# Performance work log

Measured on AMD Instinct MI355X. Metric: run time of the kernel, lower is better.

The kernel has to match this reference:

```python
import jax, jax.numpy as jnp
import numpy as np

HIDDEN_SIZE = 256
INPUT_SIZE = 4
N_CLASSES = 2


def setup_inputs() -> dict:
    key = jax.random.key(0)
    ks = jax.random.split(key, 12)
    B, T, H, I = 64, 2048, HIDDEN_SIZE, INPUT_SIZE
    s = 0.1
    return {
        "y": jax.random.normal(ks[0], (B, T), dtype=jnp.float32),
        "W_ih0": s * jax.random.normal(ks[1], (4 * H, I), dtype=jnp.float32),
        "W_hh0": s * jax.random.normal(ks[2], (4 * H, H), dtype=jnp.float32),
        "b_ih0": s * jax.random.normal(ks[3], (4 * H,), dtype=jnp.float32),
        "b_hh0": s * jax.random.normal(ks[4], (4 * H,), dtype=jnp.float32),
        "W_ih1": s * jax.random.normal(ks[5], (4 * H, H), dtype=jnp.float32),
        "W_hh1": s * jax.random.normal(ks[6], (4 * H, H), dtype=jnp.float32),
        "b_ih1": s * jax.random.normal(ks[7], (4 * H,), dtype=jnp.float32),
        "b_hh1": s * jax.random.normal(ks[8], (4 * H,), dtype=jnp.float32),
        "W_fc": s * jax.random.normal(ks[9], (N_CLASSES, H), dtype=jnp.float32),
        "b_fc": s * jax.random.normal(ks[10], (N_CLASSES,), dtype=jnp.float32),
    }


def _lstm_cell(x, h, c, Wi, Wh, bi, bh):
    # gate order i, f, g, o (torch convention, matches explicit slicing)
    gates = x @ Wi.T + bi + h @ Wh.T + bh  # [B, 4H]
    i, f, g, o = jnp.split(gates, 4, axis=-1)
    c_new = jax.nn.sigmoid(f) * c + jax.nn.sigmoid(i) * jnp.tanh(g)
    h_new = jax.nn.sigmoid(o) * jnp.tanh(c_new)
    return h_new, c_new


def reference(y, W_ih0, W_hh0, b_ih0, b_hh0, W_ih1, W_hh1, b_ih1, b_hh1, W_fc, b_fc):
    B, T = y.shape
    H = HIDDEN_SIZE
    # Sliding-window input: window [y[t-3], y[t-2], y[t-1], y[t]] with -100 pad
    padded = jnp.pad(y, ((0, 0), (0, INPUT_SIZE - 1)), constant_values=-100.0)
    seq = jnp.stack([jnp.roll(padded, s, axis=1) for s in range(INPUT_SIZE - 1, -1, -1)], axis=-1)
    seq = seq[:, :T]  # [B, T, 4]

    def step(carry, x_t):
        h0, c0, h1, c1 = carry
        h0, c0 = _lstm_cell(x_t, h0, c0, W_ih0, W_hh0, b_ih0, b_hh0)
        h1, c1 = _lstm_cell(h0, h1, c1, W_ih1, W_hh1, b_ih1, b_hh1)
        return (h0, c0, h1, c1), h1

    z = jnp.zeros((B, H), dtype=y.dtype)
    _, hs = jax.lax.scan(step, (z, z, z, z), jnp.swapaxes(seq, 0, 1))  # hs: [T, B, H]
    lstm_out = jnp.swapaxes(hs, 0, 1)  # [B, T, H]
    out = lstm_out @ W_fc.T + b_fc  # [B, T, N_CLASSES]
    return out
```

## Files before the change

kernel.cpp:

```cpp
#include <hip/hip_runtime.h>


#define NWG 64
#define NSTRIP 32
#define BB 64
#define TT 2048
#define HH 256
#define HS 8
#define HSW 4
#define RS 16

#define WS_H0    0
#define WS_H1    16384
#define WS_FLAGS 32768
#define WS_CNT   33792
#define WS_WIN   33808
#define WS_NZERO 33808

typedef float  f32x4  __attribute__((ext_vector_type(4)));
typedef __bf16 bf16x8 __attribute__((ext_vector_type(8)));
typedef unsigned long long u64;
typedef unsigned int u32;

__device__ __forceinline__ float sigf(float x)   { return 1.0f / (1.0f + __expf(-x)); }
__device__ __forceinline__ float tanh_f(float x) { return 2.0f / (1.0f + __expf(-2.0f * x)) - 1.0f; }

__global__ void init_ws(u32* ws) {
  int i = blockIdx.x * blockDim.x + threadIdx.x;
  for (; i < WS_NZERO; i += gridDim.x * blockDim.x) ws[i] = 0u;
  if (blockIdx.x == 0 && threadIdx.x == 0) ((int*)ws)[WS_WIN] = -1;
}

__global__ __launch_bounds__(256, 2) void lstm2_persistent(
    const float* __restrict__ y,
    const float* __restrict__ Wih0, const float* __restrict__ Whh0,
    const float* __restrict__ bih0, const float* __restrict__ bhh0,
    const float* __restrict__ Wih1, const float* __restrict__ Whh1,
    const float* __restrict__ bih1, const float* __restrict__ bhh1,
    const float* __restrict__ Wfc,  const float* __restrict__ bfc,
    float* __restrict__ out,
    u32* __restrict__ ws)
{
  __bf16* h0buf = (__bf16*)(ws + WS_H0);
  __bf16* h1buf = (__bf16*)(ws + WS_H1);
  int*    flags = (int*)(ws + WS_FLAGS);
  int*    cnt   = (int*)(ws + WS_CNT);
  int*    winner= (int*)(ws + WS_WIN);

  const int tid  = threadIdx.x;

  __shared__ int s_w;
  if (tid == 0) {
    int xcc = __builtin_amdgcn_s_getreg(20 | (31 << 11)) & 0xF;
    int r = atomicAdd(&cnt[xcc], 1);
    if (r == NWG - 1) atomicCAS(winner, -1, xcc);
    int wv;
    while ((wv = __hip_atomic_load(winner, __ATOMIC_RELAXED,
                                   __HIP_MEMORY_SCOPE_AGENT)) == -1) {}
    s_w = (wv == xcc && r < NWG) ? r : -1;
  }
  __syncthreads();
  const int w = s_w;
  if (w < 0) return;

  const int wave = tid >> 6;
  const int lane = tid & 63;
  const int ml   = lane & 15;
  const int kq   = lane >> 4;

  __shared__ float lds_g0[RS][BB + 4];
  __shared__ float lds_g1[RS][BB + 4];
  __shared__ float s_wih0[RS][4];
  __shared__ float s_b0[RS];
  __shared__ float s_b1[RS];

  bf16x8 w0f[8];
  bf16x8 w1f[16];
  {
    const int r     = ml;
    const int rglob = (r >> 2) * 256 + w * HSW + (r & 3);
    #pragma unroll
    for (int s = 0; s < 8; s++) {
      const float* src = Whh0 + rglob * HH + s * 32 + kq * 8;
      bf16x8 f;
      #pragma unroll
      for (int j = 0; j < 8; j++) f[j] = (__bf16)src[j];
      w0f[s] = f;
    }
    #pragma unroll
    for (int s = 0; s < 16; s++) {
      const int k = s * 32 + kq * 8;
      const float* src = (k < 256) ? (Wih1 + rglob * HH + k)
                                   : (Whh1 + rglob * HH + (k - 256));
      bf16x8 f;
      #pragma unroll
      for (int j = 0; j < 8; j++) f[j] = (__bf16)src[j];
      w1f[s] = f;
    }
  }

  if (tid < RS) {
    const int r     = tid;
    const int rglob = (r >> 2) * 256 + w * HSW + (r & 3);
    s_b0[r] = bih0[rglob] + bhh0[rglob];
    s_b1[r] = bih1[rglob] + bhh1[rglob];
    #pragma unroll
    for (int j = 0; j < 4; j++) s_wih0[r][j] = Wih0[rglob * 4 + j];
  }
  __syncthreads();

  float c0 = 0.f, c1 = 0.f;

  const int b_epi = tid >> 2;
  const int dl    = tid & 3;

  float x[4] = {-100.0f, -100.0f, -100.0f, -100.0f};

  for (int p = 0; p < TT + 2; p++) {
    const int par  = p & 1;
    const int parm = par ^ 1;

    const bool doL0 = (p < TT);
    const bool doL1 = (p >= 1 && p <= TT);

    bf16x8 a0[8], a1[8];
    {
      const int row = wave * 16 + ml;
      const __bf16* h0p = h0buf + (parm * NSTRIP * BB + kq * BB + row) * HS;
      const __bf16* h1p = h1buf + (par  * NSTRIP * BB + kq * BB + row) * HS;
      #pragma unroll
      for (int s = 0; s < 8; s++)
        asm volatile("global_load_dwordx4 %0, %1, off sc0"
                     : "=v"(a0[s]) : "v"(h0p + s * 4 * BB * HS) : "memory");
      #pragma unroll
      for (int s = 0; s < 8; s++)
        asm volatile("global_load_dwordx4 %0, %1, off sc0"
                     : "=v"(a1[s]) : "v"(h1p + s * 4 * BB * HS) : "memory");
    }

    x[0] = x[1]; x[1] = x[2]; x[2] = x[3];
    x[3] = (p < TT) ? y[b_epi * TT + p] : -100.0f;

    asm volatile("s_waitcnt vmcnt(0)" ::: "memory");
    __builtin_amdgcn_sched_barrier(0);

    f32x4 acc0  = {0.f,0.f,0.f,0.f};
    f32x4 acc1a = {0.f,0.f,0.f,0.f};
    f32x4 acc1b = {0.f,0.f,0.f,0.f};

    if (doL0) {
      #pragma unroll
      for (int s = 0; s < 8; s++)
        acc0 = __builtin_amdgcn_mfma_f32_16x16x32_bf16(a0[s], w0f[s], acc0, 0, 0, 0);
    }
    if (doL1) {
      #pragma unroll
      for (int s = 0; s < 8; s++)
        acc1a = __builtin_amdgcn_mfma_f32_16x16x32_bf16(a0[s], w1f[s], acc1a, 0, 0, 0);
      #pragma unroll
      for (int s = 0; s < 8; s++)
        acc1b = __builtin_amdgcn_mfma_f32_16x16x32_bf16(a1[s], w1f[s + 8], acc1b, 0, 0, 0);
    }

    {
      const int bb = wave * 16 + kq * 4;
      if (doL0) {
        #pragma unroll
        for (int j = 0; j < 4; j++) lds_g0[ml][bb + j] = acc0[j];
      }
      if (doL1) {
        #pragma unroll
        for (int j = 0; j < 4; j++) lds_g1[ml][bb + j] = acc1a[j] + acc1b[j];
      }
    }
    __syncthreads();

    if (doL0) {
      const float gi = lds_g0[dl     ][b_epi] + s_b0[dl     ]
        + s_wih0[dl     ][0]*x[0] + s_wih0[dl     ][1]*x[1] + s_wih0[dl     ][2]*x[2] + s_wih0[dl     ][3]*x[3];
      const float gf = lds_g0[4 + dl ][b_epi] + s_b0[4 + dl ]
        + s_wih0[4 + dl ][0]*x[0] + s_wih0[4 + dl ][1]*x[1] + s_wih0[4 + dl ][2]*x[2] + s_wih0[4 + dl ][3]*x[3];
      const float gg = lds_g0[8 + dl ][b_epi] + s_b0[8 + dl ]
        + s_wih0[8 + dl ][0]*x[0] + s_wih0[8 + dl ][1]*x[1] + s_wih0[8 + dl ][2]*x[2] + s_wih0[8 + dl ][3]*x[3];
      const float go = lds_g0[12 + dl][b_epi] + s_b0[12 + dl]
        + s_wih0[12 + dl][0]*x[0] + s_wih0[12 + dl][1]*x[1] + s_wih0[12 + dl][2]*x[2] + s_wih0[12 + dl][3]*x[3];
      const float cn = sigf(gf) * c0 + sigf(gi) * tanh_f(gg);
      c0 = cn;
      const float hn = sigf(go) * tanh_f(cn);
      h0buf[(par * NSTRIP * BB + (w >> 1) * BB + b_epi) * HS + (w & 1) * 4 + dl] = (__bf16)hn;
    }

    if (doL1) {
      const float gi = lds_g1[dl     ][b_epi] + s_b1[dl     ];
      const float gf = lds_g1[4 + dl ][b_epi] + s_b1[4 + dl ];
      const float gg = lds_g1[8 + dl ][b_epi] + s_b1[8 + dl ];
      const float go = lds_g1[12 + dl][b_epi] + s_b1[12 + dl];
      const float cn = sigf(gf) * c1 + sigf(gi) * tanh_f(gg);
      c1 = cn;
      const float hn = sigf(go) * tanh_f(cn);
      h1buf[(parm * NSTRIP * BB + (w >> 1) * BB + b_epi) * HS + (w & 1) * 4 + dl] = (__bf16)hn;
    }

    asm volatile("s_waitcnt vmcnt(0)" ::: "memory");
    __syncthreads();
    if (tid == 0)
      __hip_atomic_store(&flags[w * 16], p + 2, __ATOMIC_RELAXED,
                         __HIP_MEMORY_SCOPE_WORKGROUP);

    if (p >= 2 && wave < 2) {
      const int t = p - 2;
      const int b = w;
      const int c = wave;
      const __bf16* h1r = h1buf + (par * NSTRIP * BB + (lane >> 1) * BB + b) * HS + (lane & 1) * 4;
      union { u64 u; __bf16 h[4]; } c4;
      c4.u = __hip_atomic_load((u64*)h1r, __ATOMIC_RELAXED,
                               __HIP_MEMORY_SCOPE_AGENT);
      float s = 0.f;
      #pragma unroll
      for (int j = 0; j < 4; j++)
        s += (float)c4.h[j] * Wfc[c * HH + lane * 4 + j];
      #pragma unroll
      for (int off = 32; off > 0; off >>= 1) s += __shfl_down(s, off, 64);
      if (lane == 0) out[b * (TT * 2) + t * 2 + c] = s + bfc[c];
    }

    if (tid < NWG) {
      while (__hip_atomic_load(&flags[tid * 16], __ATOMIC_RELAXED,
                               __HIP_MEMORY_SCOPE_AGENT) < p + 2) {}
    }
    __syncthreads();
  }
}

extern "C" void kernel_launch(void* const* d_in, const int* in_sizes, int n_in,
                              void* d_out, int out_size, void* d_ws, size_t ws_size,
                              hipStream_t stream) {
  u32* ws = (u32*)d_ws;
  init_ws<<<dim3(64), dim3(256), 0, stream>>>(ws);
  lstm2_persistent<<<dim3(768), dim3(256), 0, stream>>>(
      (const float*)d_in[0],  (const float*)d_in[1], (const float*)d_in[2],
      (const float*)d_in[3],  (const float*)d_in[4], (const float*)d_in[5],
      (const float*)d_in[6],  (const float*)d_in[7], (const float*)d_in[8],
      (const float*)d_in[9],  (const float*)d_in[10],
      (float*)d_out, ws);
}
```

Measured before the change: 5.927 ms.

## Split batch across two XCDs with interleaved half-batch pipelining and per-wave flags

Rewrites the persistent LSTM so two XCDs each handle half the batch with 32 workgroups each. Within each group the batch is split into two 16-row sub-batches processed in alternating phases, so one sub-batch's synchronization latency overlaps the other's compute. Waves specialize by layer, replacing block-wide syncthreads with per-wave flags polled by whole waves. The next phase's hidden-state loads are issued right after the flag spin. This adds complexity and more flag polling traffic, and depends on getting two XCDs that each fill 32 workgroups.

```diff
diff --git a/kernel.cpp b/kernel.cpp
--- a/kernel.cpp
+++ b/kernel.cpp
@@ -1,21 +1,20 @@
 #include <hip/hip_runtime.h>
 
 
-#define NWG 64
-#define NSTRIP 32
-#define BB 64
-#define TT 2048
-#define HH 256
-#define HS 8
-#define HSW 4
-#define RS 16
+#define NWGX 32
+#define SB   16
+#define TT   2048
+#define HH   256
+#define HS   8
+#define NPH  (2*TT+4)
 
 #define WS_H0    0
 #define WS_H1    16384
 #define WS_FLAGS 32768
 #define WS_CNT   33792
-#define WS_WIN   33808
-#define WS_NZERO 33808
+#define WS_NWIN  33808
+#define WS_NZERO 33809
+#define WS_WIN   33812
 
 typedef float  f32x4  __attribute__((ext_vector_type(4)));
 typedef __bf16 bf16x8 __attribute__((ext_vector_type(8)));
@@ -25,13 +24,29 @@
 __device__ __forceinline__ float sigf(float x)   { return 1.0f / (1.0f + __expf(-x)); }
 __device__ __forceinline__ float tanh_f(float x) { return 2.0f / (1.0f + __expf(-2.0f * x)) - 1.0f; }
 
+__device__ __forceinline__ bf16x8 mk8(u64 lo, u64 hi) {
+  union { u64 u[2]; bf16x8 v; } c;
+  c.u[0] = lo; c.u[1] = hi;
+  return c.v;
+}
+
+__device__ __forceinline__ u64 ald(const void* p) {
+  return __hip_atomic_load((const u64*)p, __ATOMIC_RELAXED,
+                           __HIP_MEMORY_SCOPE_AGENT);
+}
+
+template<int N> struct ic { static constexpr int v = N; };
+
 __global__ void init_ws(u32* ws) {
   int i = blockIdx.x * blockDim.x + threadIdx.x;
   for (; i < WS_NZERO; i += gridDim.x * blockDim.x) ws[i] = 0u;
-  if (blockIdx.x == 0 && threadIdx.x == 0) ((int*)ws)[WS_WIN] = -1;
-}
-
-__global__ __launch_bounds__(256, 2) void lstm2_persistent(
+  if (blockIdx.x == 0 && threadIdx.x == 0) {
+    ((int*)ws)[WS_WIN] = -1;
+    ((int*)ws)[WS_WIN + 1] = -1;
+  }
+}
+
+__global__ __launch_bounds__(256, 1) void lstm2_persistent(
     const float* __restrict__ y,
     const float* __restrict__ Wih0, const float* __restrict__ Whh0,
     const float* __restrict__ bih0, const float* __restrict__ bhh0,
@@ -41,194 +56,248 @@
     float* __restrict__ out,
     u32* __restrict__ ws)
 {
-  __bf16* h0buf = (__bf16*)(ws + WS_H0);
-  __bf16* h1buf = (__bf16*)(ws + WS_H1);
-  int*    flags = (int*)(ws + WS_FLAGS);
-  int*    cnt   = (int*)(ws + WS_CNT);
-  int*    winner= (int*)(ws + WS_WIN);
-
-  const int tid  = threadIdx.x;
-
-  __shared__ int s_w;
+  __bf16* h0buf  = (__bf16*)(ws + WS_H0);
+  __bf16* h1buf  = (__bf16*)(ws + WS_H1);
+  int*    flags  = (int*)(ws + WS_FLAGS);
+  int*    cnt    = (int*)(ws + WS_CNT);
+  int*    nwin   = (int*)(ws + WS_NWIN);
+  int*    winners= (int*)(ws + WS_WIN);
+
+  const int tid = threadIdx.x;
+
+  __shared__ int s_w, s_g;
   if (tid == 0) {
     int xcc = __builtin_amdgcn_s_getreg(20 | (31 << 11)) & 0xF;
     int r = atomicAdd(&cnt[xcc], 1);
-    if (r == NWG - 1) atomicCAS(winner, -1, xcc);
-    int wv;
-    while ((wv = __hip_atomic_load(winner, __ATOMIC_RELAXED,
-                                   __HIP_MEMORY_SCOPE_AGENT)) == -1) {}
-    s_w = (wv == xcc && r < NWG) ? r : -1;
+    if (r == NWGX - 1) {
+      int slot = atomicAdd(nwin, 1);
+      if (slot < 2)
+        __hip_atomic_store(&winners[slot], xcc, __ATOMIC_RELAXED,
+                           __HIP_MEMORY_SCOPE_AGENT);
+    }
+    int gg = -1;
+    if (r < NWGX) {
+      int w0v, w1v;
+      do {
+        w0v = __hip_atomic_load(&winners[0], __ATOMIC_RELAXED, __HIP_MEMORY_SCOPE_AGENT);
+        w1v = __hip_atomic_load(&winners[1], __ATOMIC_RELAXED, __HIP_MEMORY_SCOPE_AGENT);
+      } while (w0v == -1 || w1v == -1);
+      if (xcc == w0v) gg = 0; else if (xcc == w1v) gg = 1;
+    }
+    s_w = r; s_g = gg;
   }
   __syncthreads();
-  const int w = s_w;
-  if (w < 0) return;
+  const int w = s_w, g = s_g;
+  if (g < 0 || w >= NWGX) return;
 
   const int wave = tid >> 6;
   const int lane = tid & 63;
+  const int ly   = wave >> 1;
+  const int nn   = wave & 1;
   const int ml   = lane & 15;
   const int kq   = lane >> 4;
-
-  __shared__ float lds_g0[RS][BB + 4];
-  __shared__ float lds_g1[RS][BB + 4];
-  __shared__ float s_wih0[RS][4];
-  __shared__ float s_b0[RS];
-  __shared__ float s_b1[RS];
-
-  bf16x8 w0f[8];
-  bf16x8 w1f[16];
+  const int bt   = lane >> 2;
+  const int dloc = lane & 3;
+
+  __shared__ float tile[4][16][20];
+
+  bf16x8 wA[16];
   {
-    const int r     = ml;
-    const int rglob = (r >> 2) * 256 + w * HSW + (r & 3);
+    const int rglob = (ml & 3) * 256 + w * HS + nn * 4 + (ml >> 2);
+    if (ly == 0) {
+      #pragma unroll
+      for (int s = 0; s < 8; s++) {
+        const float* src = Whh0 + rglob * HH + s * 32 + kq * 8;
+        bf16x8 f;
+        #pragma unroll
+        for (int j = 0; j < 8; j++) f[j] = (__bf16)src[j];
+        wA[s] = f;
+      }
+    } else {
+      #pragma unroll
+      for (int s = 0; s < 16; s++) {
+        const int k = s * 32 + kq * 8;
+        const float* src = (k < 256) ? (Wih1 + rglob * HH + k)
+                                     : (Whh1 + rglob * HH + (k - 256));
+        bf16x8 f;
+        #pragma unroll
+        for (int j = 0; j < 8; j++) f[j] = (__bf16)src[j];
+        wA[s] = f;
+      }
+    }
+  }
+
+  float bc[4];
+  float wx[4][4];
+  {
+    const int dgl = w * HS + nn * 4 + dloc;
+    #pragma unroll
+    for (int q = 0; q < 4; q++) {
+      const int rg = q * 256 + dgl;
+      if (ly == 0) {
+        bc[q] = bih0[rg] + bhh0[rg];
+        #pragma unroll
+        for (int j = 0; j < 4; j++) wx[q][j] = Wih0[rg * 4 + j];
+      } else {
+        bc[q] = bih1[rg] + bhh1[rg];
+      }
+    }
+  }
+
+  float wfc[4] = {0.f, 0.f, 0.f, 0.f};
+  float bfcv = 0.f;
+  const int fcb = w & 15;
+  const int fcc = w >> 4;
+  if (wave == 0) {
+    #pragma unroll
+    for (int j = 0; j < 4; j++) wfc[j] = Wfc[fcc * HH + lane * 4 + j];
+    bfcv = bfc[fcc];
+  }
+
+  const int aLane  = (kq * SB + ml) * HS;
+  const int pubOff = (w * SB + bt) * HS + nn * 4 + dloc;
+  const int fcOff  = ((lane >> 1) * SB + fcb) * HS + (lane & 1) * 4;
+
+  float cs0 = 0.f, cs1 = 0.f;
+  float xw0[4] = {-100.f, -100.f, -100.f, -100.f};
+  float xw1[4] = {-100.f, -100.f, -100.f, -100.f};
+  u64 a0u[16], a1u[16];
+  union { u64 u; __bf16 h[4]; } fcd; fcd.u = 0ull;
+
+  {
+    const int pr0 = 1, pr1 = 0;
+    const __bf16* a0b = h0buf + ((g * 2 + 0) * 2 + pr0) * 4096 + aLane;
     #pragma unroll
     for (int s = 0; s < 8; s++) {
-      const float* src = Whh0 + rglob * HH + s * 32 + kq * 8;
-      bf16x8 f;
-      #pragma unroll
-      for (int j = 0; j < 8; j++) f[j] = (__bf16)src[j];
-      w0f[s] = f;
-    }
-    #pragma unroll
-    for (int s = 0; s < 16; s++) {
-      const int k = s * 32 + kq * 8;
-      const float* src = (k < 256) ? (Wih1 + rglob * HH + k)
-                                   : (Whh1 + rglob * HH + (k - 256));
-      bf16x8 f;
-      #pragma unroll
-      for (int j = 0; j < 8; j++) f[j] = (__bf16)src[j];
-      w1f[s] = f;
-    }
-  }
-
-  if (tid < RS) {
-    const int r     = tid;
-    const int rglob = (r >> 2) * 256 + w * HSW + (r & 3);
-    s_b0[r] = bih0[rglob] + bhh0[rglob];
-    s_b1[r] = bih1[rglob] + bhh1[rglob];
-    #pragma unroll
-    for (int j = 0; j < 4; j++) s_wih0[r][j] = Wih0[rglob * 4 + j];
-  }
-  __syncthreads();
-
-  float c0 = 0.f, c1 = 0.f;
-
-  const int b_epi = tid >> 2;
-  const int dl    = tid & 3;
-
-  float x[4] = {-100.0f, -100.0f, -100.0f, -100.0f};
-
-  for (int p = 0; p < TT + 2; p++) {
-    const int par  = p & 1;
-    const int parm = par ^ 1;
-
-    const bool doL0 = (p < TT);
-    const bool doL1 = (p >= 1 && p <= TT);
-
-    bf16x8 a0[8], a1[8];
+      a0u[2 * s]     = ald(a0b + s * 512);
+      a0u[2 * s + 1] = ald(a0b + s * 512 + 4);
+    }
+    if (ly == 1) {
+      const __bf16* a1b = h1buf + ((g * 2 + 0) * 2 + pr1) * 4096 + aLane;
+      #pragma unroll
+      for (int s = 0; s < 8; s++) {
+        a1u[2 * s]     = ald(a1b + s * 512);
+        a1u[2 * s + 1] = ald(a1b + s * 512 + 4);
+      }
+    }
+    if (wave == 0)
+      fcd.u = ald(h1buf + ((g * 2 + 0) * 2 + 0) * 4096 + fcOff);
+  }
+
+  auto body = [&](int p, auto subc) {
+    constexpr int SUB = decltype(subc)::v;
+    const int t = p >> 1;
+    float& cst = (SUB == 0) ? cs0 : cs1;
+    float (&xw)[4] = (SUB == 0) ? xw0 : xw1;
+
+    const bool doL0w = (ly == 0) && (t < TT);
+    const bool doL1w = (ly == 1) && (t >= 1 && t <= TT);
+    const bool doFCw = (wave == 0) && (t >= 2 && t <= TT + 1);
+
+    float yv = -100.0f;
+    if (ly == 0 && t < TT) yv = y[(g * 32 + SUB * 16 + bt) * TT + t];
+
+    f32x4 acc  = {0.f, 0.f, 0.f, 0.f};
+    f32x4 accB = {0.f, 0.f, 0.f, 0.f};
+    if (doL0w) {
+      #pragma unroll
+      for (int s = 0; s < 8; s++)
+        acc = __builtin_amdgcn_mfma_f32_16x16x32_bf16(
+            mk8(a0u[2 * s], a0u[2 * s + 1]), wA[s], acc, 0, 0, 0);
+    }
+    if (doL1w) {
+      #pragma unroll
+      for (int s = 0; s < 8; s++)
+        acc  = __builtin_amdgcn_mfma_f32_16x16x32_bf16(
+            mk8(a0u[2 * s], a0u[2 * s + 1]), wA[s],     acc,  0, 0, 0);
+      #pragma unroll
+      for (int s = 0; s < 8; s++)
+        accB = __builtin_amdgcn_mfma_f32_16x16x32_bf16(
+            mk8(a1u[2 * s], a1u[2 * s + 1]), wA[s + 8], accB, 0, 0, 0);
+    }
+
+    if (doL0w || doL1w) {
+      f32x4 sum = acc + accB;
+      *(f32x4*)&tile[wave][ml][kq * 4] = sum;
+    }
+    asm volatile("s_waitcnt lgkmcnt(0)" ::: "memory");
+
+    if (doL0w) {
+      xw[0] = xw[1]; xw[1] = xw[2]; xw[2] = xw[3]; xw[3] = yv;
+      float gv[4];
+      #pragma unroll
+      for (int q = 0; q < 4; q++)
+        gv[q] = tile[wave][dloc * 4 + q][bt] + bc[q]
+              + wx[q][0] * xw[0] + wx[q][1] * xw[1]
+              + wx[q][2] * xw[2] + wx[q][3] * xw[3];
+      const float cn = sigf(gv[1]) * cst + sigf(gv[0]) * tanh_f(gv[2]);
+      cst = cn;
+      const float hn = sigf(gv[3]) * tanh_f(cn);
+      h0buf[((g * 2 + SUB) * 2 + (t & 1)) * 4096 + pubOff] = (__bf16)hn;
+    }
+    if (doL1w) {
+      float gv[4];
+      #pragma unroll
+      for (int q = 0; q < 4; q++)
+        gv[q] = tile[wave][dloc * 4 + q][bt] + bc[q];
+      const float cn = sigf(gv[1]) * cst + sigf(gv[0]) * tanh_f(gv[2]);
+      cst = cn;
+      const float hn = sigf(gv[3]) * tanh_f(cn);
+      h1buf[((g * 2 + SUB) * 2 + ((t - 1) & 1)) * 4096 + pubOff] = (__bf16)hn;
+    }
+
+    if (doFCw) {
+      float s = 0.f;
+      #pragma unroll
+      for (int j = 0; j < 4; j++) s += (float)fcd.h[j] * wfc[j];
+      #pragma unroll
+      for (int off = 32; off > 0; off >>= 1) s += __shfl_down(s, off, 64);
+      if (lane == 0)
+        out[(g * 32 + SUB * 16 + fcb) * (TT * 2) + (t - 2) * 2 + fcc] = s + bfcv;
+    }
+
     {
-      const int row = wave * 16 + ml;
-      const __bf16* h0p = h0buf + (parm * NSTRIP * BB + kq * BB + row) * HS;
-      const __bf16* h1p = h1buf + (par  * NSTRIP * BB + kq * BB + row) * HS;
-      #pragma unroll
-      for (int s = 0; s < 8; s++)
-        asm volatile("global_load_dwordx4 %0, %1, off sc0"
-                     : "=v"(a0[s]) : "v"(h0p + s * 4 * BB * HS) : "memory");
-      #pragma unroll
-      for (int s = 0; s < 8; s++)
-        asm volatile("global_load_dwordx4 %0, %1, off sc0"
-                     : "=v"(a1[s]) : "v"(h1p + s * 4 * BB * HS) : "memory");
-    }
-
-    x[0] = x[1]; x[1] = x[2]; x[2] = x[3];
-    x[3] = (p < TT) ? y[b_epi * TT + p] : -100.0f;
+      int* f0 = &flags[(g * 128 + lane) * 4];
+      int* f1 = &flags[(g * 128 + 64 + lane) * 4];
+      int a, b;
+      do {
+        a = __hip_atomic_load(f0, __ATOMIC_RELAXED, __HIP_MEMORY_SCOPE_AGENT);
+        b = __hip_atomic_load(f1, __ATOMIC_RELAXED, __HIP_MEMORY_SCOPE_AGENT);
+      } while (!__all((a < b ? a : b) >= p));
+    }
 
     asm volatile("s_waitcnt vmcnt(0)" ::: "memory");
-    __builtin_amdgcn_sched_barrier(0);
-
-    f32x4 acc0  = {0.f,0.f,0.f,0.f};
-    f32x4 acc1a = {0.f,0.f,0.f,0.f};
-    f32x4 acc1b = {0.f,0.f,0.f,0.f};
-
-    if (doL0) {
-      #pragma unroll
-      for (int s = 0; s < 8; s++)
-        acc0 = __builtin_amdgcn_mfma_f32_16x16x32_bf16(a0[s], w0f[s], acc0, 0, 0, 0);
-    }
-    if (doL1) {
-      #pragma unroll
-      for (int s = 0; s < 8; s++)
-        acc1a = __builtin_amdgcn_mfma_f32_16x16x32_bf16(a0[s], w1f[s], acc1a, 0, 0, 0);
-      #pragma unroll
-      for (int s = 0; s < 8; s++)
-        acc1b = __builtin_amdgcn_mfma_f32_16x16x32_bf16(a1[s], w1f[s + 8], acc1b, 0, 0, 0);
-    }
+    if (lane == 0)
+      __hip_atomic_store(&flags[(g * 128 + w * 4 + wave) * 4], p + 1,
+                         __ATOMIC_RELAXED, __HIP_MEMORY_SCOPE_WORKGROUP);
 
     {
-      const int bb = wave * 16 + kq * 4;
-      if (doL0) {
+      const int tn  = (p + 1) >> 1;
+      constexpr int SUBN = SUB ^ 1;
+      const int pr0 = (tn - 1) & 1;
+      const int pr1 = tn & 1;
+      const __bf16* a0b = h0buf + ((g * 2 + SUBN) * 2 + pr0) * 4096 + aLane;
+      #pragma unroll
+      for (int s = 0; s < 8; s++) {
+        a0u[2 * s]     = ald(a0b + s * 512);
+        a0u[2 * s + 1] = ald(a0b + s * 512 + 4);
+      }
+      if (ly == 1) {
+        const __bf16* a1b = h1buf + ((g * 2 + SUBN) * 2 + pr1) * 4096 + aLane;
         #pragma unroll
-        for (int j = 0; j < 4; j++) lds_g0[ml][bb + j] = acc0[j];
-      }
-      if (doL1) {
-        #pragma unroll
-        for (int j = 0; j < 4; j++) lds_g1[ml][bb + j] = acc1a[j] + acc1b[j];
-      }
-    }
-    __syncthreads();
-
-    if (doL0) {
-      const float gi = lds_g0[dl     ][b_epi] + s_b0[dl     ]
-        + s_wih0[dl     ][0]*x[0] + s_wih0[dl     ][1]*x[1] + s_wih0[dl     ][2]*x[2] + s_wih0[dl     ][3]*x[3];
-      const float gf = lds_g0[4 + dl ][b_epi] + s_b0[4 + dl ]
-        + s_wih0[4 + dl ][0]*x[0] + s_wih0[4 + dl ][1]*x[1] + s_wih0[4 + dl ][2]*x[2] + s_wih0[4 + dl ][3]*x[3];
-      const float gg = lds_g0[8 + dl ][b_epi] + s_b0[8 + dl ]
-        + s_wih0[8 + dl ][0]*x[0] + s_wih0[8 + dl ][1]*x[1] + s_wih0[8 + dl ][2]*x[2] + s_wih0[8 + dl ][3]*x[3];
-      const float go = lds_g0[12 + dl][b_epi] + s_b0[12 + dl]
-        + s_wih0[12 + dl][0]*x[0] + s_wih0[12 + dl][1]*x[1] + s_wih0[12 + dl][2]*x[2] + s_wih0[12 + dl][3]*x[3];
-      const float cn = sigf(gf) * c0 + sigf(gi) * tanh_f(gg);
-      c0 = cn;
-      const float hn = sigf(go) * tanh_f(cn);
-      h0buf[(par * NSTRIP * BB + (w >> 1) * BB + b_epi) * HS + (w & 1) * 4 + dl] = (__bf16)hn;
-    }
-
-    if (doL1) {
-      const float gi = lds_g1[dl     ][b_epi] + s_b1[dl     ];
-      const float gf = lds_g1[4 + dl ][b_epi] + s_b1[4 + dl ];
-      const float gg = lds_g1[8 + dl ][b_epi] + s_b1[8 + dl ];
-      const float go = lds_g1[12 + dl][b_epi] + s_b1[12 + dl];
-      const float cn = sigf(gf) * c1 + sigf(gi) * tanh_f(gg);
-      c1 = cn;
-      const float hn = sigf(go) * tanh_f(cn);
-      h1buf[(parm * NSTRIP * BB + (w >> 1) * BB + b_epi) * HS + (w & 1) * 4 + dl] = (__bf16)hn;
-    }
-
-    asm volatile("s_waitcnt vmcnt(0)" ::: "memory");
-    __syncthreads();
-    if (tid == 0)
-      __hip_atomic_store(&flags[w * 16], p + 2, __ATOMIC_RELAXED,
-                         __HIP_MEMORY_SCOPE_WORKGROUP);
-
-    if (p >= 2 && wave < 2) {
-      const int t = p - 2;
-      const int b = w;
-      const int c = wave;
-      const __bf16* h1r = h1buf + (par * NSTRIP * BB + (lane >> 1) * BB + b) * HS + (lane & 1) * 4;
-      union { u64 u; __bf16 h[4]; } c4;
-      c4.u = __hip_atomic_load((u64*)h1r, __ATOMIC_RELAXED,
-                               __HIP_MEMORY_SCOPE_AGENT);
-      float s = 0.f;
-      #pragma unroll
-      for (int j = 0; j < 4; j++)
-        s += (float)c4.h[j] * Wfc[c * HH + lane * 4 + j];
-      #pragma unroll
-      for (int off = 32; off > 0; off >>= 1) s += __shfl_down(s, off, 64);
-      if (lane == 0) out[b * (TT * 2) + t * 2 + c] = s + bfc[c];
-    }
-
-    if (tid < NWG) {
-      while (__hip_atomic_load(&flags[tid * 16], __ATOMIC_RELAXED,
-                               __HIP_MEMORY_SCOPE_AGENT) < p + 2) {}
-    }
-    __syncthreads();
+        for (int s = 0; s < 8; s++) {
+          a1u[2 * s]     = ald(a1b + s * 512);
+          a1u[2 * s + 1] = ald(a1b + s * 512 + 4);
+        }
+      }
+      if (wave == 0)
+        fcd.u = ald(h1buf + ((g * 2 + SUBN) * 2 + (tn & 1)) * 4096 + fcOff);
+    }
+  };
+
+  for (int ph = 0; ph < NPH; ph += 2) {
+    body(ph,     ic<0>{});
+    body(ph + 1, ic<1>{});
   }
 }
 
```

After: 8.306 ms. 1.4x slower.
